# Kernel tuning notes

Hardware: AMD Instinct MI355X
Metric: run time of the kernel (lower is better)

Reference implementation:

```python
import jax, jax.numpy as jnp
import numpy as np
from jax import lax

B, C, H, W = 4, 64, 256, 320
PT = 6
EPS = 1e-6
BN_EPS = 1e-5


def conv2d(x, w, b=None):
    y = lax.conv_general_dilated(x, w, (1, 1), 'SAME',
                                 dimension_numbers=('NCHW', 'OIHW', 'NCHW'))
    if b is not None:
        y = y + b[None, :, None, None]
    return y


def batchnorm(x, g, b):
    # training-mode batch statistics over (N, H, W)
    m = jnp.mean(x, axis=(0, 2, 3), keepdims=True)
    v = jnp.var(x, axis=(0, 2, 3), keepdims=True)
    return g[None, :, None, None] * (x - m) * lax.rsqrt(v + BN_EPS) + b[None, :, None, None]


def gen_kernel(fout, wconv, g, b, pk):
    # Basic2d: conv(no bias) -> BN -> ReLU, producing pk*pk-1 affinity channels
    w = jax.nn.relu(batchnorm(conv2d(fout, wconv), g, b))
    s = jnp.sum(jnp.abs(w), axis=1, keepdims=True)
    w = w / (s + EPS)
    mid = 1.0 - jnp.sum(w, axis=1, keepdims=True)
    h = (pk * pk - 1) // 2
    return jnp.concatenate([w[:, :h], mid, w[:, h:]], axis=1)  # [B, pk*pk, H, W]


def spatial_kernel(d, sigma):
    r = jnp.linspace(-1.0, 1.0, d)
    x, y = jnp.meshgrid(r, r, indexing='ij')
    return jnp.exp(-(x * x + y * y) / (2.0 * sigma * sigma)).reshape(1, d * d, 1, 1)


def local_conv(x, w, pk):
    # per-pixel spatially-varying conv: x [B,1,H,W], w [B,pk*pk,H,W]
    patches = lax.conv_general_dilated_patches(
        x, (pk, pk), (1, 1), 'SAME', dimension_numbers=('NCHW', 'OIHW', 'NCHW'))
    return jnp.sum(patches * w, axis=1, keepdims=True)


def setup_inputs() -> dict:
    key = jax.random.key(0)
    ks = jax.random.split(key, 16)
    f32 = jnp.float32
    inp = {
        'fout': jax.random.normal(ks[0], (B, C, H, W), f32),
        'hn': jax.random.uniform(ks[1], (B, 1, H, W), f32),
        'h0': jax.random.uniform(ks[2], (B, 1, H, W), f32),
        # GenKernel_L convs (no bias, followed by BN)
        'w3_conv': jax.random.normal(ks[3], (8, C, 3, 3), f32) * 0.05,
        'w3_g': jnp.ones((8,), f32), 'w3_b': jnp.zeros((8,), f32),
        'w5_conv': jax.random.normal(ks[4], (24, C, 3, 3), f32) * 0.05,
        'w5_g': jnp.ones((24,), f32), 'w5_b': jnp.zeros((24,), f32),
        'w7_conv': jax.random.normal(ks[5], (48, C, 3, 3), f32) * 0.05,
        'w7_g': jnp.ones((48,), f32), 'w7_b': jnp.zeros((48,), f32),
        # confidence heads (conv with bias -> softmax over channels)
        'ck_w': jax.random.normal(ks[6], (3, C, 3, 3), f32) * 0.05,
        'ck_b': jnp.zeros((3,), f32),
        'ct_w': jax.random.normal(ks[7], (3, C + 3, 3, 3), f32) * 0.05,
        'ct_b': jnp.zeros((3,), f32),
        'sig3': jnp.float32(1.0), 'sig5': jnp.float32(1.0), 'sig7': jnp.float32(1.0),
    }
    return inp


def reference(fout, hn, h0, w3_conv, w3_g, w3_b, w5_conv, w5_g, w5_b,
              w7_conv, w7_g, w7_b, ck_w, ck_b, ct_w, ct_b, sig3, sig5, sig7):
    weight3 = gen_kernel(fout, w3_conv, w3_g, w3_b, 3) * spatial_kernel(3, sig3)
    weight5 = gen_kernel(fout, w5_conv, w5_g, w5_b, 5) * spatial_kernel(5, sig5)
    weight7 = gen_kernel(fout, w7_conv, w7_g, w7_b, 7) * spatial_kernel(7, sig7)
    weight3 = weight3 / jnp.clip(jnp.sum(weight3, 1, keepdims=True), 1e-7)
    weight5 = weight5 / jnp.clip(jnp.sum(weight5, 1, keepdims=True), 1e-7)
    weight7 = weight7 / jnp.clip(jnp.sum(weight7, 1, keepdims=True), 1e-7)

    confk = jax.nn.softmax(conv2d(fout, ck_w, ck_b), axis=1)
    conf3, conf5, conf7 = confk[:, 0:1], confk[:, 1:2], confk[:, 2:3]

    hn3 = hn5 = hn7 = hn
    hns = [hn]
    for i in range(PT):
        hn3 = local_conv(hn3, weight3, 3)
        hn5 = local_conv(hn5, weight5, 5)
        hn7 = local_conv(hn7, weight7, 7)
        if i == PT // 2 - 1:
            hns.append(conf3 * hn3 + conf5 * hn5 + conf7 * hn7)
    hns.append(conf3 * hn3 + conf5 * hn5 + conf7 * hn7)
    hns = jnp.concatenate(hns, axis=1)  # [B, 3, H, W]

    wt = jax.nn.softmax(conv2d(jnp.concatenate([fout, hns], axis=1), ct_w, ct_b), axis=1)
    return jnp.sum(wt * hns, axis=1, keepdims=True)
```

## Files before the change

### kernel.cpp

```cpp
#include <hip/hip_runtime.h>
#include <hip/hip_bf16.h>
#include <math.h>

#define W_    320
#define H_    256
#define HW_   81920
#define BHW_  327680
#define PRM_TOT 49786

#define OW3  0
#define OW5  4608
#define OW7  18432
#define OCK  46080
#define OCT  47808
#define OG3  49617
#define OB3  49625
#define OG5  49633
#define OB5  49657
#define OG7  49681
#define OB7  49729
#define OCKB 49777
#define OCTB 49780
#define OSIG 49783

typedef unsigned short u16;
typedef __attribute__((ext_vector_type(8))) short short8;
typedef __attribute__((ext_vector_type(4))) float f32x4;

__device__ __forceinline__ float dload(const void* p, size_t i, int isbf) {
  return isbf ? __bfloat162float(((const __hip_bfloat16*)p)[i])
              : ((const float*)p)[i];
}

__device__ __forceinline__ u16 f32_bf16_rne(float f) {
  union { float f; unsigned u; } v; v.f = f;
  unsigned r = v.u + 0x7FFFu + ((v.u >> 16) & 1u);
  return (u16)(r >> 16);
}
__device__ __forceinline__ float bf16_f32(u16 h) {
  union { unsigned u; float f; } v; v.u = ((unsigned)h) << 16;
  return v.f;
}

__device__ __forceinline__ unsigned wquant(float w) {
  int v = (int)(w * 65536.f + 0.5f);
  return (unsigned)(v > 65535 ? 65535 : (v < 0 ? 0 : v));
}

__global__ __launch_bounds__(512) void k_detect(
    const void* t0, const void* t1, const void* t2, const void* t3,
    const void* t4, const void* t5, const void* t6, const void* t7,
    const void* t8, const void* t9, const void* t10, const void* t11,
    const void* t12, const void* t13, const void* t14, const void* t15,
    const void* t16, const void* t17, int* __restrict__ flags)
{
  __shared__ int c_other, c_zeven, c_zodd, c_m;
  const void* ptrs[18] = {t0,t1,t2,t3,t4,t5,t6,t7,t8,t9,
                          t10,t11,t12,t13,t14,t15,t16,t17};
  const int ns[18] = {20971520, 327680, 4608, 8, 8, 13824, 24, 24,
                      27648, 48, 48, 1728, 3, 1809, 3, 1, 1, 1};
  const int tensor = blockIdx.x;
  const int n = ns[tensor];
  const unsigned short* u = (const unsigned short*)ptrs[tensor];
  if (threadIdx.x == 0) { c_other = 0; c_zeven = 0; c_zodd = 0; c_m = 0; }
  __syncthreads();
  {
    int k = threadIdx.x >> 1;
    long long pos = (long long)k * n / 256;
    int j = ((int)pos & ~1) + (threadIdx.x & 1);
    if (j < n) {
      unsigned short v = u[j];
      int e = (v >> 7) & 0xFF;
      atomicAdd(&c_m, 1);
      if (v != 0 && (e < 90 || e > 150)) atomicAdd(&c_other, 1);
      if (v == 0) {
        if (j & 1) atomicAdd(&c_zodd, 1); else atomicAdd(&c_zeven, 1);
      }
    }
  }
  __syncthreads();
  if (threadIdx.x == 0) {
    int isf32;
    if (n == 1) isf32 = (u[0] == 0);
    else        isf32 = (4 * c_other >= c_m) ||
                        (2 * (c_zeven - c_zodd) >= c_m);
    flags[tensor] = isf32 ? 0 : 1;
  }
}

__global__ __launch_bounds__(256) void k_cvt(
    const void* w3c, const void* w5c, const void* w7c, const void* ckw, const void* ctw,
    const void* g3, const void* b3, const void* g5, const void* b5,
    const void* g7, const void* b7, const void* ckb, const void* ctb,
    const void* s3, const void* s5, const void* s7,
    float* __restrict__ prm, const int* __restrict__ flags)
{
  int j = blockIdx.x * 256 + threadIdx.x;
  if (j >= PRM_TOT) return;
  const void* src; int off; int fid;
  if      (j < OW5)    { src = w3c; off = OW3;  fid = 2; }
  else if (j < OW7)    { src = w5c; off = OW5;  fid = 5; }
  else if (j < OCK)    { src = w7c; off = OW7;  fid = 8; }
  else if (j < OCT)    { src = ckw; off = OCK;  fid = 11; }
  else if (j < OG3)    { src = ctw; off = OCT;  fid = 13; }
  else if (j < OB3)    { src = g3;  off = OG3;  fid = 3; }
  else if (j < OG5)    { src = b3;  off = OB3;  fid = 4; }
  else if (j < OB5)    { src = g5;  off = OG5;  fid = 6; }
  else if (j < OG7)    { src = b5;  off = OB5;  fid = 7; }
  else if (j < OB7)    { src = g7;  off = OG7;  fid = 9; }
  else if (j < OCKB)   { src = b7;  off = OB7;  fid = 10; }
  else if (j < OCTB)   { src = ckb; off = OCKB; fid = 12; }
  else if (j < OSIG)   { src = ctb; off = OCTB; fid = 14; }
  else if (j < OSIG+1) { src = s3;  off = OSIG;   fid = 15; }
  else if (j < OSIG+2) { src = s5;  off = OSIG+1; fid = 16; }
  else                 { src = s7;  off = OSIG+2; fid = 17; }
  prm[j] = dload(src, j - off, flags[fid]);
}

__global__ __launch_bounds__(256) void k_pack(
    const float* __restrict__ prm, u16* __restrict__ apack)
{
  int idx = blockIdx.x * 256 + threadIdx.x;
  int e = idx & 7;
  int lane = (idx >> 3) & 63;
  int t = idx >> 9;
  int mt = t % 6; t /= 6;
  int chunk = t & 1; t >>= 1;
  int tap = t % 9;
  int hilo = t / 9;
  int oc = mt * 16 + (lane & 15);
  int ic = chunk * 32 + (lane >> 4) * 8 + e;
  float w = (oc < 83) ? prm[(size_t)oc * 576 + (size_t)ic * 9 + tap] : 0.f;
  u16 h = f32_bf16_rne(w);
  u16 outv = (hilo == 0) ? h : f32_bf16_rne(w - bf16_f32(h));
  apack[idx] = outv;
}

template<int ISBF>
__device__ __forceinline__ void stage_chunk(
    const void* __restrict__ fout, int b, int y0, int x0, int chunk,
    u16* Bhi, u16* Blo)
{
  const int g = threadIdx.x & 3;
  const int cell0 = threadIdx.x >> 2;
  const size_t fb = (size_t)b * 64 * HW_ + (size_t)(chunk * 32 + g * 8) * HW_;
#pragma unroll
  for (int it = 0; it < 7; ++it) {
    int cell = cell0 + it * 64;
    if (cell < 396) {
      int row = cell / 66;
      int px = cell - row * 66;
      int gy = y0 - 1 + row, gx = x0 - 1 + px;
      bool ok = ((unsigned)gy < H_) && ((unsigned)gx < W_);
      size_t base = fb + (size_t)gy * W_ + gx;
      short8 hs = {0,0,0,0,0,0,0,0};
      short8 ls = {0,0,0,0,0,0,0,0};
#pragma unroll
      for (int i = 0; i < 8; ++i) {
        float v = ok ? dload(fout, base + (size_t)i * HW_, ISBF) : 0.f;
        union { float f; unsigned u; } uv; uv.f = v;
        u16 h = (u16)(uv.u >> 16);
        float resid = v - bf16_f32(h);
        hs[i] = (short)h;
        ls[i] = (short)f32_bf16_rne(resid);
      }
      int off = ((row * 66 + px) * 32 + g * 8) * 2;
      off ^= (px & 7) << 4;
      *(short8*)((char*)Bhi + off) = hs;
      *(short8*)((char*)Blo + off) = ls;
    }
  }
}

__global__ __launch_bounds__(256, 2) void k_conv_mfma(
    const void* __restrict__ fout, const u16* __restrict__ apack,
    float* __restrict__ wbuf, float* __restrict__ stat,
    const int* __restrict__ flags)
{
  __shared__ __align__(16) u16 Bhi[6 * 66 * 32];
  __shared__ __align__(16) u16 Blo[6 * 66 * 32];
  const int isbf = flags[0];
  const int x0 = blockIdx.x * 64;
  const int y0 = blockIdx.y * 4;
  const int b  = blockIdx.z;
  const int lane = threadIdx.x & 63;
  const int wv   = threadIdx.x >> 6;

  const f32x4 zero = {0.f, 0.f, 0.f, 0.f};
  f32x4 acc[6][4];
#pragma unroll
  for (int mt = 0; mt < 6; ++mt)
#pragma unroll
    for (int nt = 0; nt < 4; ++nt)
      acc[mt][nt] = zero;

  for (int chunk = 0; chunk < 2; ++chunk) {
    if (chunk) __syncthreads();
    if (isbf) stage_chunk<1>(fout, b, y0, x0, chunk, Bhi, Blo);
    else      stage_chunk<0>(fout, b, y0, x0, chunk, Bhi, Blo);
    __syncthreads();

#pragma unroll
    for (int tap = 0; tap < 9; ++tap) {
      const int dy = tap / 3, dx = tap - dy * 3;
      const int row = wv + dy;
      short8 bh[4], bl[4];
#pragma unroll
      for (int nt = 0; nt < 4; ++nt) {
        int px = nt * 16 + (lane & 15) + dx;
        int off = ((row * 66 + px) * 32 + (lane >> 4) * 8) * 2;
        off ^= (px & 7) << 4;
        bh[nt] = *(const short8*)((const char*)Bhi + off);
        bl[nt] = *(const short8*)((const char*)Blo + off);
      }
      const u16* abase = apack + (size_t)(tap * 2 + chunk) * 3072 + (size_t)lane * 8;
#pragma unroll
      for (int mt = 0; mt < 6; ++mt) {
        short8 ah = *(const short8*)(abase + (size_t)mt * 512);
        short8 al = *(const short8*)(abase + (size_t)mt * 512 + 55296);
#pragma unroll
        for (int nt = 0; nt < 4; ++nt) {
          acc[mt][nt] = __builtin_amdgcn_mfma_f32_16x16x32_bf16(ah, bh[nt], acc[mt][nt], 0, 0, 0);
          acc[mt][nt] = __builtin_amdgcn_mfma_f32_16x16x32_bf16(ah, bl[nt], acc[mt][nt], 0, 0, 0);
          acc[mt][nt] = __builtin_amdgcn_mfma_f32_16x16x32_bf16(al, bh[nt], acc[mt][nt], 0, 0, 0);
        }
      }
    }
  }

  const int ocr = (lane >> 4) * 4;
  const size_t rowoff = (size_t)(y0 + wv) * W_ + x0 + (lane & 15);
#pragma unroll
  for (int mt = 0; mt < 6; ++mt) {
#pragma unroll
    for (int nt = 0; nt < 4; ++nt) {
#pragma unroll
      for (int r = 0; r < 4; ++r) {
        int oc = mt * 16 + ocr + r;
        if (oc < 83)
          wbuf[((size_t)b * 83 + oc) * HW_ + rowoff + nt * 16] = acc[mt][nt][r];
      }
    }
  }

  __syncthreads();
  float* sm = (float*)Bhi;
  if (threadIdx.x < 192) sm[threadIdx.x] = 0.f;
  __syncthreads();
#pragma unroll
  for (int mt = 0; mt < 6; ++mt) {
#pragma unroll
    for (int r = 0; r < 4; ++r) {
      float s = 0.f, qq = 0.f;
#pragma unroll
      for (int nt = 0; nt < 4; ++nt) { float a = acc[mt][nt][r]; s += a; qq += a * a; }
#pragma unroll
      for (int m = 1; m < 16; m <<= 1) {
        s  += __shfl_xor(s, m, 64);
        qq += __shfl_xor(qq, m, 64);
      }
      if ((lane & 15) == 0) {
        int oc = mt * 16 + ocr + r;
        atomicAdd(&sm[oc], s);
        atomicAdd(&sm[96 + oc], qq);
      }
    }
  }
  __syncthreads();
  if (threadIdx.x < 80) {
    atomicAdd(&stat[threadIdx.x], sm[threadIdx.x]);
    atomicAdd(&stat[80 + threadIdx.x], sm[96 + threadIdx.x]);
  }
}

__global__ void k_bn_finalize(float* __restrict__ stat)
{
  int ch = threadIdx.x;
  if (ch < 80) {
    const float n = 1.f / (float)BHW_;
    float m = stat[ch] * n;
    float var = stat[80 + ch] * n - m * m;
    stat[160 + ch] = m;
    stat[240 + ch] = rsqrtf(var + 1e-5f);
  }
}

__global__ __launch_bounds__(256, 2) void k_prop0(
    float* __restrict__ wbuf, float* __restrict__ conf,
    const void* __restrict__ rawhn,
    float* __restrict__ h3o, float* __restrict__ h5o, float* __restrict__ h7o,
    const float* __restrict__ prm, const float* __restrict__ stat,
    const int* __restrict__ flags)
{
  const int isbf = flags[1];
  const int p = blockIdx.x * 256 + threadIdx.x;
  const int b = p / HW_, q = p - b * HW_;
  const int y = q / W_, x = q - y * W_;
  const size_t bo = (size_t)b * HW_;
  float* base = wbuf + ((size_t)b * 83) * HW_ + q;

  float cv[83];
#pragma unroll
  for (int ch = 0; ch < 83; ++ch) cv[ch] = base[(size_t)ch * HW_];

  {
    float c0 = cv[80] + prm[OCKB + 0];
    float c1 = cv[81] + prm[OCKB + 1];
    float c2 = cv[82] + prm[OCKB + 2];
    float m = fmaxf(c0, fmaxf(c1, c2));
    float e0 = expf(c0 - m), e1 = expf(c1 - m), e2 = expf(c2 - m);
    float inv = 1.f / (e0 + e1 + e2);
    float* cf = conf + ((size_t)b * 3) * HW_ + q;
    cf[0] = e0 * inv;
    cf[(size_t)HW_] = e1 * inv;
    cf[(size_t)2 * HW_] = e2 * inv;
  }

  const float* mean = stat + 160;
  const float* istd = stat + 240;
#pragma unroll
  for (int ch = 0; ch < 8; ++ch)
    cv[ch] = fmaxf(0.f, (cv[ch] - mean[ch]) * istd[ch] * prm[OG3 + ch] + prm[OB3 + ch]);
#pragma unroll
  for (int ch = 0; ch < 24; ++ch)
    cv[8 + ch] = fmaxf(0.f, (cv[8 + ch] - mean[8 + ch]) * istd[8 + ch] * prm[OG5 + ch] + prm[OB5 + ch]);
#pragma unroll
  for (int ch = 0; ch < 48; ++ch)
    cv[32 + ch] = fmaxf(0.f, (cv[32 + ch] - mean[32 + ch]) * istd[32 + ch] * prm[OG7 + ch] + prm[OB7 + ch]);

  float kout[83];

  {
    float s = 0.f;
#pragma unroll
    for (int i = 0; i < 8; ++i) s += cv[i];
    float inv = 1.f / (s + 1e-6f);
    float wn[8]; float sn = 0.f;
#pragma unroll
    for (int i = 0; i < 8; ++i) { wn[i] = cv[i] * inv; sn += wn[i]; }
    float kk[9];
#pragma unroll
    for (int j = 0; j < 4; ++j) kk[j] = wn[j];
    kk[4] = 1.f - sn;
#pragma unroll
    for (int j = 0; j < 4; ++j) kk[5 + j] = wn[4 + j];
    float sg = prm[OSIG + 0];
    float a = 0.5f / (sg * sg);
    float e1 = expf(-a);
    float g1[3] = {e1, 1.f, e1};
    float tot = 0.f;
#pragma unroll
    for (int j = 0; j < 9; ++j) { kk[j] *= g1[j / 3] * g1[j % 3]; tot += kk[j]; }
    float rr = 1.f / fmaxf(tot, 1e-7f);
#pragma unroll
    for (int j = 0; j < 9; ++j) kout[j] = kk[j] * rr;
  }
  {
    float s = 0.f;
#pragma unroll
    for (int i = 0; i < 24; ++i) s += cv[8 + i];
    float inv = 1.f / (s + 1e-6f);
    float wn[24]; float sn = 0.f;
#pragma unroll
    for (int i = 0; i < 24; ++i) { wn[i] = cv[8 + i] * inv; sn += wn[i]; }
    float kk[25];
#pragma unroll
    for (int j = 0; j < 12; ++j) kk[j] = wn[j];
    kk[12] = 1.f - sn;
#pragma unroll
    for (int j = 0; j < 12; ++j) kk[13 + j] = wn[12 + j];
    float sg = prm[OSIG + 1];
    float a = 0.5f / (sg * sg);
    float ea = expf(-a), eb = expf(-0.25f * a);
    float g1[5] = {ea, eb, 1.f, eb, ea};
    float tot = 0.f;
#pragma unroll
    for (int j = 0; j < 25; ++j) { kk[j] *= g1[j / 5] * g1[j % 5]; tot += kk[j]; }
    float rr = 1.f / fmaxf(tot, 1e-7f);
#pragma unroll
    for (int j = 0; j < 25; ++j) kout[9 + j] = kk[j] * rr;
  }
  {
    float s = 0.f;
#pragma unroll
    for (int i = 0; i < 48; ++i) s += cv[32 + i];
    float inv = 1.f / (s + 1e-6f);
    float wn[48]; float sn = 0.f;
#pragma unroll
    for (int i = 0; i < 48; ++i) { wn[i] = cv[32 + i] * inv; sn += wn[i]; }
    float kk[49];
#pragma unroll
    for (int j = 0; j < 24; ++j) kk[j] = wn[j];
    kk[24] = 1.f - sn;
#pragma unroll
    for (int j = 0; j < 24; ++j) kk[25 + j] = wn[24 + j];
    float sg = prm[OSIG + 2];
    float a = 0.5f / (sg * sg);
    float ea = expf(-a), eb = expf(-(4.f / 9.f) * a), ec = expf(-(1.f / 9.f) * a);
    float g1[7] = {ea, eb, ec, 1.f, ec, eb, ea};
    float tot = 0.f;
#pragma unroll
    for (int j = 0; j < 49; ++j) { kk[j] *= g1[j / 7] * g1[j % 7]; tot += kk[j]; }
    float rr = 1.f / fmaxf(tot, 1e-7f);
#pragma unroll
    for (int j = 0; j < 49; ++j) kout[34 + j] = kk[j] * rr;
  }

#pragma unroll
  for (int pr = 0; pr < 42; ++pr) {
    unsigned u0 = wquant(kout[2 * pr]);
    unsigned u1 = (2 * pr + 1 < 83) ? wquant(kout[2 * pr + 1]) : 0u;
    unsigned pkv = u0 | (u1 << 16);
    base[(size_t)pr * HW_] = __uint_as_float(pkv);
  }

  float a3 = 0.f, a5 = 0.f, a7 = 0.f;
#pragma unroll
  for (int j = 0; j < 9; ++j) {
    int gy = y + j / 3 - 1, gx = x + j % 3 - 1;
    float v = 0.f;
    if ((unsigned)gy < H_ && (unsigned)gx < W_)
      v = dload(rawhn, bo + (size_t)gy * W_ + gx, isbf);
    a3 = fmaf(kout[j], v, a3);
  }
#pragma unroll
  for (int j = 0; j < 25; ++j) {
    int gy = y + j / 5 - 2, gx = x + j % 5 - 2;
    float v = 0.f;
    if ((unsigned)gy < H_ && (unsigned)gx < W_)
      v = dload(rawhn, bo + (size_t)gy * W_ + gx, isbf);
    a5 = fmaf(kout[9 + j], v, a5);
  }
#pragma unroll
  for (int j = 0; j < 49; ++j) {
    int gy = y + j / 7 - 3, gx = x + j % 7 - 3;
    float v = 0.f;
    if ((unsigned)gy < H_ && (unsigned)gx < W_)
      v = dload(rawhn, bo + (size_t)gy * W_ + gx, isbf);
    a7 = fmaf(kout[34 + j], v, a7);
  }
  h3o[bo + q] = a3;
  h5o[bo + q] = a5;
  h7o[bo + q] = a7;
}

__global__ __launch_bounds__(256) void k_prop_q(
    const float* __restrict__ wbuf, const float* __restrict__ conf,
    const float* __restrict__ h3i, const float* __restrict__ h5i,
    const float* __restrict__ h7i,
    float* __restrict__ h3o, float* __restrict__ h5o, float* __restrict__ h7o,
    float* __restrict__ combo, int store_h)
{
  const int p = blockIdx.x * 256 + threadIdx.x;
  const int b = p / HW_, q = p - b * HW_;
  const int y = q / W_, x = q - y * W_;
  const size_t bo = (size_t)b * HW_;
  const float* base = wbuf + ((size_t)b * 83) * HW_ + q;

  unsigned pk[42];
#pragma unroll
  for (int pr = 0; pr < 42; ++pr)
    pk[pr] = __float_as_uint(base[(size_t)pr * HW_]);
  const float sc = 1.f / 65536.f;
#define WDEC(CH) ((float)((pk[(CH) >> 1] >> (((CH) & 1) * 16)) & 0xffffu) * sc)

  float a3 = 0.f, a5 = 0.f, a7 = 0.f;
#pragma unroll
  for (int j = 0; j < 9; ++j) {
    int gy = y + j / 3 - 1, gx = x + j % 3 - 1;
    float v = 0.f;
    if ((unsigned)gy < H_ && (unsigned)gx < W_)
      v = h3i[bo + (size_t)gy * W_ + gx];
    a3 = fmaf(WDEC(j), v, a3);
  }
#pragma unroll
  for (int j = 0; j < 25; ++j) {
    int gy = y + j / 5 - 2, gx = x + j % 5 - 2;
    float v = 0.f;
    if ((unsigned)gy < H_ && (unsigned)gx < W_)
      v = h5i[bo + (size_t)gy * W_ + gx];
    a5 = fmaf(WDEC(9 + j), v, a5);
  }
#pragma unroll
  for (int j = 0; j < 49; ++j) {
    int gy = y + j / 7 - 3, gx = x + j % 7 - 3;
    float v = 0.f;
    if ((unsigned)gy < H_ && (unsigned)gx < W_)
      v = h7i[bo + (size_t)gy * W_ + gx];
    a7 = fmaf(WDEC(34 + j), v, a7);
  }
#undef WDEC
  if (store_h) {
    h3o[bo + q] = a3;
    h5o[bo + q] = a5;
    h7o[bo + q] = a7;
  }
  if (combo) {
    const float* cf = conf + ((size_t)b * 3) * HW_ + q;
    combo[bo + q] = cf[0] * a3 + cf[(size_t)HW_] * a5 + cf[(size_t)2 * HW_] * a7;
  }
}

__global__ __launch_bounds__(256, 2) void k_final(
    const void* __restrict__ fout, const void* __restrict__ rawhn,
    const float* __restrict__ mid, const float* __restrict__ fin,
    const float* __restrict__ prm, float* __restrict__ out,
    const int* __restrict__ flags)
{
  const int isbf_f = flags[0];
  const int isbf_h = flags[1];
  const float* ctw = prm + OCT;
  const int p = blockIdx.x * 256 + threadIdx.x;
  const int b = p / HW_, q = p - b * HW_;
  const int y = q / W_, x = q - y * W_;
  const size_t bo = (size_t)b * HW_;

  int toff[9]; bool tok[9];
#pragma unroll
  for (int j = 0; j < 9; ++j) {
    int gy = y + j / 3 - 1, gx = x + j % 3 - 1;
    tok[j] = (unsigned)gy < H_ && (unsigned)gx < W_;
    toff[j] = gy * W_ + gx;
  }
  const size_t fbase = (size_t)b * 64 * HW_;

  float l0 = prm[OCTB + 0], l1 = prm[OCTB + 1], l2 = prm[OCTB + 2];

  for (int ic = 0; ic < 64; ++ic) {
#pragma unroll
    for (int j = 0; j < 9; ++j) {
      float v = tok[j] ? dload(fout, fbase + (size_t)ic * HW_ + toff[j], isbf_f) : 0.f;
      l0 = fmaf(v, ctw[(0 * 67 + ic) * 9 + j], l0);
      l1 = fmaf(v, ctw[(1 * 67 + ic) * 9 + j], l1);
      l2 = fmaf(v, ctw[(2 * 67 + ic) * 9 + j], l2);
    }
  }
#pragma unroll
  for (int c = 0; c < 3; ++c) {
    const int icg = 64 + c;
#pragma unroll
    for (int j = 0; j < 9; ++j) {
      int gy = y + j / 3 - 1, gx = x + j % 3 - 1;
      float v = 0.f;
      if ((unsigned)gy < H_ && (unsigned)gx < W_) {
        size_t gi = bo + (size_t)gy * W_ + gx;
        v = (c == 0) ? dload(rawhn, gi, isbf_h) : (c == 1) ? mid[gi] : fin[gi];
      }
      l0 = fmaf(v, ctw[(0 * 67 + icg) * 9 + j], l0);
      l1 = fmaf(v, ctw[(1 * 67 + icg) * 9 + j], l1);
      l2 = fmaf(v, ctw[(2 * 67 + icg) * 9 + j], l2);
    }
  }
  float m = fmaxf(l0, fmaxf(l1, l2));
  float e0 = expf(l0 - m), e1 = expf(l1 - m), e2 = expf(l2 - m);
  float inv = 1.f / (e0 + e1 + e2);
  float h0c = dload(rawhn, bo + q, isbf_h);
  float r = (e0 * h0c + e1 * mid[bo + q] + e2 * fin[bo + q]) * inv;
  out[bo + q] = r;
}

extern "C" void kernel_launch(void* const* d_in, const int* in_sizes, int n_in,
                              void* d_out, int out_size, void* d_ws, size_t ws_size,
                              hipStream_t stream)
{
  static const int EXP[19] = {20971520, 327680, 327680, 4608, 8, 8, 13824, 24, 24,
                              27648, 48, 48, 1728, 3, 1809, 3, 1, 1, 1};
  const void* P[19];
  bool match = (n_in >= 19);
  for (int i = 0; i < 19 && match; ++i) if (in_sizes[i] != EXP[i]) match = false;
  if (match) {
    for (int i = 0; i < 19; ++i) P[i] = d_in[i];
  } else {
    bool used[64] = {false};
    for (int t = 0; t < 19; ++t) {
      P[t] = d_in[t < n_in ? t : 0];
      for (int i = 0; i < n_in && i < 64; ++i)
        if (!used[i] && in_sizes[i] == EXP[t]) { P[t] = d_in[i]; used[i] = true; break; }
    }
  }
  const void* fout = P[0];
  const void* hn   = P[1];
  float* out = (float*)d_out;

  float* ws    = (float*)d_ws;
  int*   flags = (int*)ws;
  float* stat  = ws + 32;
  float* prm   = ws + 352;
  float* big   = ws + 50176;
  float* wbuf  = big;
  float* conf  = wbuf + (size_t)83 * BHW_;
  float* hnA   = conf + (size_t)3 * BHW_;
  float* hnB   = hnA + (size_t)3 * BHW_;
  float* midb  = hnB + (size_t)3 * BHW_;
  float* finb  = midb + (size_t)BHW_;
  u16*   apack = (u16*)midb;

  (void)hipMemsetAsync(stat, 0, 160 * sizeof(float), stream);

  k_detect<<<18, 512, 0, stream>>>(
      P[0], P[1], P[3], P[4], P[5], P[6], P[7], P[8],
      P[9], P[10], P[11], P[12], P[13], P[14], P[15],
      P[16], P[17], P[18], flags);

  k_cvt<<<(PRM_TOT + 255) / 256, 256, 0, stream>>>(
      P[3], P[6], P[9], P[12], P[14],
      P[4], P[5], P[7], P[8], P[10], P[11],
      P[13], P[15], P[16], P[17], P[18], prm, flags);

  k_pack<<<432, 256, 0, stream>>>(prm, apack);
  k_conv_mfma<<<dim3(5, 64, 4), 256, 0, stream>>>(fout, apack, wbuf, stat, flags);
  k_bn_finalize<<<1, 128, 0, stream>>>(stat);

  k_prop0<<<1280, 256, 0, stream>>>(
      wbuf, conf, hn, hnA, hnA + (size_t)BHW_, hnA + (size_t)2 * BHW_,
      prm, stat, flags);

  const float* i3 = hnA;
  const float* i5 = hnA + (size_t)BHW_;
  const float* i7 = hnA + (size_t)2 * BHW_;
  for (int it = 1; it < 6; ++it) {
    float* base = (it & 1) ? hnB : hnA;
    float* o3 = base;
    float* o5 = base + (size_t)BHW_;
    float* o7 = base + (size_t)2 * BHW_;
    float* combo = (it == 2) ? midb : (it == 5) ? finb : nullptr;
    k_prop_q<<<1280, 256, 0, stream>>>(
        wbuf, conf, i3, i5, i7, o3, o5, o7, combo, (it < 5) ? 1 : 0);
    i3 = o3; i5 = o5; i7 = o7;
  }

  k_final<<<1280, 256, 0, stream>>>(fout, hn, midb, finb, prm, out, flags);
}
```

Measured before the change: 490.2 us.

## Fold final conv's fout part into MFMA conv, split waves, deterministic BN stats

Packs the three fout-channel weights of the final confidence conv into the spare MFMA output rows (83..85). Their logits are written to a separate buffer, so k_final no longer recomputes a 64-channel 3x3 scalar conv from fout. The MFMA conv block grows to 512 threads, with each wave half covering three of the six M-tiles. The BN statistics path replaces global atomics with per-block partial sums reduced by a new kernel. k_prop0 also drops its 83-float register arrays in favour of per-group streaming to ease register pressure. The fused-logit path depends on workspace size and falls back to the old code when space is short.

```diff
diff --git a/kernel.cpp b/kernel.cpp
--- a/kernel.cpp
+++ b/kernel.cpp
@@ -130,7 +130,9 @@
   int hilo = t / 9;
   int oc = mt * 16 + (lane & 15);
   int ic = chunk * 32 + (lane >> 4) * 8 + e;
-  float w = (oc < 83) ? prm[(size_t)oc * 576 + (size_t)ic * 9 + tap] : 0.f;
+  float w = 0.f;
+  if (oc < 83)      w = prm[(size_t)oc * 576 + (size_t)ic * 9 + tap];
+  else if (oc < 86) w = prm[OCT + (size_t)((oc - 83) * 67 + ic) * 9 + tap];
   u16 h = f32_bf16_rne(w);
   u16 outv = (hilo == 0) ? h : f32_bf16_rne(w - bf16_f32(h));
   apack[idx] = outv;
@@ -145,8 +147,8 @@
   const int cell0 = threadIdx.x >> 2;
   const size_t fb = (size_t)b * 64 * HW_ + (size_t)(chunk * 32 + g * 8) * HW_;
 #pragma unroll
-  for (int it = 0; it < 7; ++it) {
-    int cell = cell0 + it * 64;
+  for (int it = 0; it < 4; ++it) {
+    int cell = cell0 + it * 128;
     if (cell < 396) {
       int row = cell / 66;
       int px = cell - row * 66;
@@ -172,10 +174,10 @@
   }
 }
 
-__global__ __launch_bounds__(256, 2) void k_conv_mfma(
+__global__ __launch_bounds__(512, 4) void k_conv_mfma(
     const void* __restrict__ fout, const u16* __restrict__ apack,
-    float* __restrict__ wbuf, float* __restrict__ stat,
-    const int* __restrict__ flags)
+    float* __restrict__ wbuf, float* __restrict__ logit,
+    float* __restrict__ partial, const int* __restrict__ flags)
 {
   __shared__ __align__(16) u16 Bhi[6 * 66 * 32];
   __shared__ __align__(16) u16 Blo[6 * 66 * 32];
@@ -185,11 +187,13 @@
   const int b  = blockIdx.z;
   const int lane = threadIdx.x & 63;
   const int wv   = threadIdx.x >> 6;
+  const int wrow = wv & 3;
+  const int half = wv >> 2;
 
   const f32x4 zero = {0.f, 0.f, 0.f, 0.f};
-  f32x4 acc[6][4];
-#pragma unroll
-  for (int mt = 0; mt < 6; ++mt)
+  f32x4 acc[3][4];
+#pragma unroll
+  for (int mt = 0; mt < 3; ++mt)
 #pragma unroll
     for (int nt = 0; nt < 4; ++nt)
       acc[mt][nt] = zero;
@@ -203,7 +207,7 @@
 #pragma unroll
     for (int tap = 0; tap < 9; ++tap) {
       const int dy = tap / 3, dx = tap - dy * 3;
-      const int row = wv + dy;
+      const int row = wrow + dy;
       short8 bh[4], bl[4];
 #pragma unroll
       for (int nt = 0; nt < 4; ++nt) {
@@ -213,9 +217,10 @@
         bh[nt] = *(const short8*)((const char*)Bhi + off);
         bl[nt] = *(const short8*)((const char*)Blo + off);
       }
-      const u16* abase = apack + (size_t)(tap * 2 + chunk) * 3072 + (size_t)lane * 8;
-#pragma unroll
-      for (int mt = 0; mt < 6; ++mt) {
+      const u16* abase = apack + (size_t)(tap * 2 + chunk) * 3072
+                               + (size_t)(half * 3) * 512 + (size_t)lane * 8;
+#pragma unroll
+      for (int mt = 0; mt < 3; ++mt) {
         short8 ah = *(const short8*)(abase + (size_t)mt * 512);
         short8 al = *(const short8*)(abase + (size_t)mt * 512 + 55296);
 #pragma unroll
@@ -229,16 +234,18 @@
   }
 
   const int ocr = (lane >> 4) * 4;
-  const size_t rowoff = (size_t)(y0 + wv) * W_ + x0 + (lane & 15);
-#pragma unroll
-  for (int mt = 0; mt < 6; ++mt) {
+  const size_t rowoff = (size_t)(y0 + wrow) * W_ + x0 + (lane & 15);
+#pragma unroll
+  for (int mt = 0; mt < 3; ++mt) {
 #pragma unroll
     for (int nt = 0; nt < 4; ++nt) {
 #pragma unroll
       for (int r = 0; r < 4; ++r) {
-        int oc = mt * 16 + ocr + r;
+        int oc = (half * 3 + mt) * 16 + ocr + r;
         if (oc < 83)
           wbuf[((size_t)b * 83 + oc) * HW_ + rowoff + nt * 16] = acc[mt][nt][r];
+        else if (oc < 86 && logit)
+          logit[((size_t)b * 3 + (oc - 83)) * HW_ + rowoff + nt * 16] = acc[mt][nt][r];
       }
     }
   }
@@ -248,7 +255,7 @@
   if (threadIdx.x < 192) sm[threadIdx.x] = 0.f;
   __syncthreads();
 #pragma unroll
-  for (int mt = 0; mt < 6; ++mt) {
+  for (int mt = 0; mt < 3; ++mt) {
 #pragma unroll
     for (int r = 0; r < 4; ++r) {
       float s = 0.f, qq = 0.f;
@@ -260,28 +267,40 @@
         qq += __shfl_xor(qq, m, 64);
       }
       if ((lane & 15) == 0) {
-        int oc = mt * 16 + ocr + r;
+        int oc = (half * 3 + mt) * 16 + ocr + r;
         atomicAdd(&sm[oc], s);
         atomicAdd(&sm[96 + oc], qq);
       }
     }
   }
   __syncthreads();
-  if (threadIdx.x < 80) {
-    atomicAdd(&stat[threadIdx.x], sm[threadIdx.x]);
-    atomicAdd(&stat[80 + threadIdx.x], sm[96 + threadIdx.x]);
-  }
-}
-
-__global__ void k_bn_finalize(float* __restrict__ stat)
-{
-  int ch = threadIdx.x;
-  if (ch < 80) {
+  const int blk = blockIdx.x + 5 * (blockIdx.y + 64 * blockIdx.z);
+  if (threadIdx.x < 160)
+    partial[(size_t)blk * 160 + threadIdx.x] =
+        (threadIdx.x < 80) ? sm[threadIdx.x] : sm[threadIdx.x + 16];
+}
+
+__global__ __launch_bounds__(256) void k_bn_reduce(
+    const float* __restrict__ partial, float* __restrict__ stat)
+{
+  const int half = threadIdx.x >> 7;
+  const int ch = blockIdx.x + half * 80;
+  float acc = 0.f;
+  for (int i = (threadIdx.x & 127); i < 1280; i += 128)
+    acc += partial[(size_t)i * 160 + ch];
+#pragma unroll
+  for (int m = 1; m < 64; m <<= 1) acc += __shfl_xor(acc, m, 64);
+  __shared__ float r[4];
+  if ((threadIdx.x & 63) == 0) r[threadIdx.x >> 6] = acc;
+  __syncthreads();
+  if (threadIdx.x == 0) {
+    float s  = r[0] + r[1];
+    float qq = r[2] + r[3];
     const float n = 1.f / (float)BHW_;
-    float m = stat[ch] * n;
-    float var = stat[80 + ch] * n - m * m;
-    stat[160 + ch] = m;
-    stat[240 + ch] = rsqrtf(var + 1e-5f);
+    float m = s * n;
+    float var = qq * n - m * m;
+    stat[160 + blockIdx.x] = m;
+    stat[240 + blockIdx.x] = rsqrtf(var + 1e-5f);
   }
 }
 
@@ -298,15 +317,19 @@
   const int y = q / W_, x = q - y * W_;
   const size_t bo = (size_t)b * HW_;
   float* base = wbuf + ((size_t)b * 83) * HW_ + q;
-
-  float cv[83];
-#pragma unroll
-  for (int ch = 0; ch < 83; ++ch) cv[ch] = base[(size_t)ch * HW_];
+  const float* mean = stat + 160;
+  const float* istd = stat + 240;
+
+  auto hload = [&](int gy, int gx) -> float {
+    if ((unsigned)gy < H_ && (unsigned)gx < W_)
+      return dload(rawhn, bo + (size_t)gy * W_ + gx, isbf);
+    return 0.f;
+  };
 
   {
-    float c0 = cv[80] + prm[OCKB + 0];
-    float c1 = cv[81] + prm[OCKB + 1];
-    float c2 = cv[82] + prm[OCKB + 2];
+    float c0 = base[(size_t)80 * HW_] + prm[OCKB + 0];
+    float c1 = base[(size_t)81 * HW_] + prm[OCKB + 1];
+    float c2 = base[(size_t)82 * HW_] + prm[OCKB + 2];
     float m = fmaxf(c0, fmaxf(c1, c2));
     float e0 = expf(c0 - m), e1 = expf(c1 - m), e2 = expf(c2 - m);
     float inv = 1.f / (e0 + e1 + e2);
@@ -316,129 +339,120 @@
     cf[(size_t)2 * HW_] = e2 * inv;
   }
 
-  const float* mean = stat + 160;
-  const float* istd = stat + 240;
-#pragma unroll
-  for (int ch = 0; ch < 8; ++ch)
-    cv[ch] = fmaxf(0.f, (cv[ch] - mean[ch]) * istd[ch] * prm[OG3 + ch] + prm[OB3 + ch]);
-#pragma unroll
-  for (int ch = 0; ch < 24; ++ch)
-    cv[8 + ch] = fmaxf(0.f, (cv[8 + ch] - mean[8 + ch]) * istd[8 + ch] * prm[OG5 + ch] + prm[OB5 + ch]);
-#pragma unroll
-  for (int ch = 0; ch < 48; ++ch)
-    cv[32 + ch] = fmaxf(0.f, (cv[32 + ch] - mean[32 + ch]) * istd[32 + ch] * prm[OG7 + ch] + prm[OB7 + ch]);
-
-  float kout[83];
+  float a3, a5, a7;
+  unsigned carry;
 
   {
-    float s = 0.f;
-#pragma unroll
-    for (int i = 0; i < 8; ++i) s += cv[i];
+    float cvv[8]; float s = 0.f;
+#pragma unroll
+    for (int i = 0; i < 8; ++i) {
+      float v = base[(size_t)i * HW_];
+      v = fmaxf(0.f, (v - mean[i]) * istd[i] * prm[OG3 + i] + prm[OB3 + i]);
+      cvv[i] = v; s += v;
+    }
     float inv = 1.f / (s + 1e-6f);
-    float wn[8]; float sn = 0.f;
-#pragma unroll
-    for (int i = 0; i < 8; ++i) { wn[i] = cv[i] * inv; sn += wn[i]; }
-    float kk[9];
-#pragma unroll
-    for (int j = 0; j < 4; ++j) kk[j] = wn[j];
-    kk[4] = 1.f - sn;
-#pragma unroll
-    for (int j = 0; j < 4; ++j) kk[5 + j] = wn[4 + j];
+    float ctr = 1.f - s * inv;
     float sg = prm[OSIG + 0];
     float a = 0.5f / (sg * sg);
     float e1 = expf(-a);
     float g1[3] = {e1, 1.f, e1};
     float tot = 0.f;
 #pragma unroll
-    for (int j = 0; j < 9; ++j) { kk[j] *= g1[j / 3] * g1[j % 3]; tot += kk[j]; }
+    for (int j = 0; j < 9; ++j) {
+      float w = (j == 4) ? ctr : cvv[j < 4 ? j : j - 1] * inv;
+      w *= g1[j / 3] * g1[j % 3];
+      if (j == 4) ctr = w; else cvv[j < 4 ? j : j - 1] = w;
+      tot += w;
+    }
     float rr = 1.f / fmaxf(tot, 1e-7f);
-#pragma unroll
-    for (int j = 0; j < 9; ++j) kout[j] = kk[j] * rr;
-  }
+    auto wk = [&](int c) -> float {
+      return ((c == 4) ? ctr : cvv[c < 4 ? c : c - 1]) * rr;
+    };
+    a3 = 0.f;
+#pragma unroll
+    for (int j = 0; j < 9; ++j)
+      a3 = fmaf(wk(j), hload(y + j / 3 - 1, x + j % 3 - 1), a3);
+#pragma unroll
+    for (int pr = 0; pr < 4; ++pr)
+      base[(size_t)pr * HW_] =
+          __uint_as_float(wquant(wk(2 * pr)) | (wquant(wk(2 * pr + 1)) << 16));
+    carry = wquant(wk(8));
+  }
+
   {
-    float s = 0.f;
-#pragma unroll
-    for (int i = 0; i < 24; ++i) s += cv[8 + i];
+    float cvv[24]; float s = 0.f;
+#pragma unroll
+    for (int i = 0; i < 24; ++i) {
+      float v = base[(size_t)(8 + i) * HW_];
+      v = fmaxf(0.f, (v - mean[8 + i]) * istd[8 + i] * prm[OG5 + i] + prm[OB5 + i]);
+      cvv[i] = v; s += v;
+    }
     float inv = 1.f / (s + 1e-6f);
-    float wn[24]; float sn = 0.f;
-#pragma unroll
-    for (int i = 0; i < 24; ++i) { wn[i] = cv[8 + i] * inv; sn += wn[i]; }
-    float kk[25];
-#pragma unroll
-    for (int j = 0; j < 12; ++j) kk[j] = wn[j];
-    kk[12] = 1.f - sn;
-#pragma unroll
-    for (int j = 0; j < 12; ++j) kk[13 + j] = wn[12 + j];
+    float ctr = 1.f - s * inv;
     float sg = prm[OSIG + 1];
     float a = 0.5f / (sg * sg);
     float ea = expf(-a), eb = expf(-0.25f * a);
     float g1[5] = {ea, eb, 1.f, eb, ea};
     float tot = 0.f;
 #pragma unroll
-    for (int j = 0; j < 25; ++j) { kk[j] *= g1[j / 5] * g1[j % 5]; tot += kk[j]; }
+    for (int j = 0; j < 25; ++j) {
+      float w = (j == 12) ? ctr : cvv[j < 12 ? j : j - 1] * inv;
+      w *= g1[j / 5] * g1[j % 5];
+      if (j == 12) ctr = w; else cvv[j < 12 ? j : j - 1] = w;
+      tot += w;
+    }
     float rr = 1.f / fmaxf(tot, 1e-7f);
-#pragma unroll
-    for (int j = 0; j < 25; ++j) kout[9 + j] = kk[j] * rr;
-  }
+    auto wk = [&](int j) -> float {
+      return ((j == 12) ? ctr : cvv[j < 12 ? j : j - 1]) * rr;
+    };
+    a5 = 0.f;
+#pragma unroll
+    for (int j = 0; j < 25; ++j)
+      a5 = fmaf(wk(j), hload(y + j / 5 - 2, x + j % 5 - 2), a5);
+    base[(size_t)4 * HW_] = __uint_as_float(carry | (wquant(wk(0)) << 16));
+#pragma unroll
+    for (int m = 0; m < 12; ++m)
+      base[(size_t)(5 + m) * HW_] =
+          __uint_as_float(wquant(wk(1 + 2 * m)) | (wquant(wk(2 + 2 * m)) << 16));
+  }
+
   {
-    float s = 0.f;
-#pragma unroll
-    for (int i = 0; i < 48; ++i) s += cv[32 + i];
+    float cvv[48]; float s = 0.f;
+#pragma unroll
+    for (int i = 0; i < 48; ++i) {
+      float v = base[(size_t)(32 + i) * HW_];
+      v = fmaxf(0.f, (v - mean[32 + i]) * istd[32 + i] * prm[OG7 + i] + prm[OB7 + i]);
+      cvv[i] = v; s += v;
+    }
     float inv = 1.f / (s + 1e-6f);
-    float wn[48]; float sn = 0.f;
-#pragma unroll
-    for (int i = 0; i < 48; ++i) { wn[i] = cv[32 + i] * inv; sn += wn[i]; }
-    float kk[49];
-#pragma unroll
-    for (int j = 0; j < 24; ++j) kk[j] = wn[j];
-    kk[24] = 1.f - sn;
-#pragma unroll
-    for (int j = 0; j < 24; ++j) kk[25 + j] = wn[24 + j];
+    float ctr = 1.f - s * inv;
     float sg = prm[OSIG + 2];
     float a = 0.5f / (sg * sg);
     float ea = expf(-a), eb = expf(-(4.f / 9.f) * a), ec = expf(-(1.f / 9.f) * a);
     float g1[7] = {ea, eb, ec, 1.f, ec, eb, ea};
     float tot = 0.f;
 #pragma unroll
-    for (int j = 0; j < 49; ++j) { kk[j] *= g1[j / 7] * g1[j % 7]; tot += kk[j]; }
+    for (int j = 0; j < 49; ++j) {
+      float w = (j == 24) ? ctr : cvv[j < 24 ? j : j - 1] * inv;
+      w *= g1[j / 7] * g1[j % 7];
+      if (j == 24) ctr = w; else cvv[j < 24 ? j : j - 1] = w;
+      tot += w;
+    }
     float rr = 1.f / fmaxf(tot, 1e-7f);
-#pragma unroll
-    for (int j = 0; j < 49; ++j) kout[34 + j] = kk[j] * rr;
-  }
-
-#pragma unroll
-  for (int pr = 0; pr < 42; ++pr) {
-    unsigned u0 = wquant(kout[2 * pr]);
-    unsigned u1 = (2 * pr + 1 < 83) ? wquant(kout[2 * pr + 1]) : 0u;
-    unsigned pkv = u0 | (u1 << 16);
-    base[(size_t)pr * HW_] = __uint_as_float(pkv);
-  }
-
-  float a3 = 0.f, a5 = 0.f, a7 = 0.f;
-#pragma unroll
-  for (int j = 0; j < 9; ++j) {
-    int gy = y + j / 3 - 1, gx = x + j % 3 - 1;
-    float v = 0.f;
-    if ((unsigned)gy < H_ && (unsigned)gx < W_)
-      v = dload(rawhn, bo + (size_t)gy * W_ + gx, isbf);
-    a3 = fmaf(kout[j], v, a3);
-  }
-#pragma unroll
-  for (int j = 0; j < 25; ++j) {
-    int gy = y + j / 5 - 2, gx = x + j % 5 - 2;
-    float v = 0.f;
-    if ((unsigned)gy < H_ && (unsigned)gx < W_)
-      v = dload(rawhn, bo + (size_t)gy * W_ + gx, isbf);
-    a5 = fmaf(kout[9 + j], v, a5);
-  }
-#pragma unroll
-  for (int j = 0; j < 49; ++j) {
-    int gy = y + j / 7 - 3, gx = x + j % 7 - 3;
-    float v = 0.f;
-    if ((unsigned)gy < H_ && (unsigned)gx < W_)
-      v = dload(rawhn, bo + (size_t)gy * W_ + gx, isbf);
-    a7 = fmaf(kout[34 + j], v, a7);
-  }
+    auto wk = [&](int j) -> float {
+      return ((j == 24) ? ctr : cvv[j < 24 ? j : j - 1]) * rr;
+    };
+    a7 = 0.f;
+#pragma unroll
+    for (int j = 0; j < 49; ++j)
+      a7 = fmaf(wk(j), hload(y + j / 7 - 3, x + j % 7 - 3), a7);
+#pragma unroll
+    for (int m = 0; m < 24; ++m)
+      base[(size_t)(17 + m) * HW_] =
+          __uint_as_float(wquant(wk(2 * m)) | (wquant(wk(2 * m + 1)) << 16));
+    base[(size_t)41 * HW_] = __uint_as_float(wquant(wk(48)));
+  }
+
   h3o[bo + q] = a3;
   h5o[bo + q] = a5;
   h7o[bo + q] = a7;
@@ -504,6 +518,7 @@
 __global__ __launch_bounds__(256, 2) void k_final(
     const void* __restrict__ fout, const void* __restrict__ rawhn,
     const float* __restrict__ mid, const float* __restrict__ fin,
+    const float* __restrict__ logit,
     const float* __restrict__ prm, float* __restrict__ out,
     const int* __restrict__ flags)
 {
@@ -515,26 +530,33 @@
   const int y = q / W_, x = q - y * W_;
   const size_t bo = (size_t)b * HW_;
 
-  int toff[9]; bool tok[9];
-#pragma unroll
-  for (int j = 0; j < 9; ++j) {
-    int gy = y + j / 3 - 1, gx = x + j % 3 - 1;
-    tok[j] = (unsigned)gy < H_ && (unsigned)gx < W_;
-    toff[j] = gy * W_ + gx;
-  }
-  const size_t fbase = (size_t)b * 64 * HW_;
-
   float l0 = prm[OCTB + 0], l1 = prm[OCTB + 1], l2 = prm[OCTB + 2];
 
-  for (int ic = 0; ic < 64; ++ic) {
+  if (logit) {
+    const float* lg = logit + ((size_t)b * 3) * HW_ + q;
+    l0 += lg[0];
+    l1 += lg[(size_t)HW_];
+    l2 += lg[(size_t)2 * HW_];
+  } else {
+    int toff[9]; bool tok[9];
 #pragma unroll
     for (int j = 0; j < 9; ++j) {
-      float v = tok[j] ? dload(fout, fbase + (size_t)ic * HW_ + toff[j], isbf_f) : 0.f;
-      l0 = fmaf(v, ctw[(0 * 67 + ic) * 9 + j], l0);
-      l1 = fmaf(v, ctw[(1 * 67 + ic) * 9 + j], l1);
-      l2 = fmaf(v, ctw[(2 * 67 + ic) * 9 + j], l2);
-    }
-  }
+      int gy = y + j / 3 - 1, gx = x + j % 3 - 1;
+      tok[j] = (unsigned)gy < H_ && (unsigned)gx < W_;
+      toff[j] = gy * W_ + gx;
+    }
+    const size_t fbase = (size_t)b * 64 * HW_;
+    for (int ic = 0; ic < 64; ++ic) {
+#pragma unroll
+      for (int j = 0; j < 9; ++j) {
+        float v = tok[j] ? dload(fout, fbase + (size_t)ic * HW_ + toff[j], isbf_f) : 0.f;
+        l0 = fmaf(v, ctw[(0 * 67 + ic) * 9 + j], l0);
+        l1 = fmaf(v, ctw[(1 * 67 + ic) * 9 + j], l1);
+        l2 = fmaf(v, ctw[(2 * 67 + ic) * 9 + j], l2);
+      }
+    }
+  }
+
 #pragma unroll
   for (int c = 0; c < 3; ++c) {
     const int icg = 64 + c;
@@ -594,8 +616,9 @@
   float* midb  = hnB + (size_t)3 * BHW_;
   float* finb  = midb + (size_t)BHW_;
   u16*   apack = (u16*)midb;
-
-  (void)hipMemsetAsync(stat, 0, 160 * sizeof(float), stream);
+  float* partial = hnA;
+  size_t need = ((size_t)50176 + (size_t)97 * BHW_) * sizeof(float);
+  float* logitb = (ws_size >= need) ? (finb + (size_t)BHW_) : nullptr;
 
   k_detect<<<18, 512, 0, stream>>>(
       P[0], P[1], P[3], P[4], P[5], P[6], P[7], P[8],
@@ -608,8 +631,9 @@
       P[13], P[15], P[16], P[17], P[18], prm, flags);
 
   k_pack<<<432, 256, 0, stream>>>(prm, apack);
-  k_conv_mfma<<<dim3(5, 64, 4), 256, 0, stream>>>(fout, apack, wbuf, stat, flags);
-  k_bn_finalize<<<1, 128, 0, stream>>>(stat);
+  k_conv_mfma<<<dim3(5, 64, 4), 512, 0, stream>>>(fout, apack, wbuf, logitb,
+                                                  partial, flags);
+  k_bn_reduce<<<80, 256, 0, stream>>>(partial, stat);
 
   k_prop0<<<1280, 256, 0, stream>>>(
       wbuf, conf, hn, hnA, hnA + (size_t)BHW_, hnA + (size_t)2 * BHW_,
@@ -629,5 +653,5 @@
     i3 = o3; i5 = o5; i7 = o7;
   }
 
-  k_final<<<1280, 256, 0, stream>>>(fout, hn, midb, finb, prm, out, flags);
-}
+  k_final<<<1280, 256, 0, stream>>>(fout, hn, midb, finb, logitb, prm, out, flags);
+}
```

Result: faster. 453.5 us (-7.5%).
